# Performance work log

Measured on AMD Instinct MI355X. Metric: run time of the kernel, lower is better.

Reference implementation:

```python
import jax, jax.numpy as jnp
import numpy as np

N_GRAPHS = 64

def setup_inputs() -> dict:
    key = jax.random.key(0)
    ks = jax.random.split(key, 8)
    N, E, H = 50000, 600000, 128
    x = jax.random.normal(ks[0], (N, 2), dtype=jnp.float32)
    edge_index = jax.random.randint(ks[1], (2, E), 0, N, dtype=jnp.int64)
    batch = jnp.sort(jax.random.randint(ks[2], (N,), 0, N_GRAPHS, dtype=jnp.int64))
    s = 0.1  # keep tanh out of saturation
    return {
        'x': x,
        'edge_index': edge_index,
        'batch': batch,
        'W1': jax.random.normal(ks[3], (2, H), dtype=jnp.float32) * s,
        'b1': jnp.zeros((H,), jnp.float32),
        'W2': jax.random.normal(ks[4], (H, H), dtype=jnp.float32) * s,
        'b2': jnp.zeros((H,), jnp.float32),
        'W3': jax.random.normal(ks[5], (H, H), dtype=jnp.float32) * s,
        'b3': jnp.zeros((H,), jnp.float32),
        'Wo': jax.random.normal(ks[6], (2 * H, 41), dtype=jnp.float32) * s,
        'bo': jnp.zeros((41,), jnp.float32),
    }

def reference(x, edge_index, batch, W1, b1, W2, b2, W3, b3, Wo, bo):
    N = x.shape[0]
    src, dst = edge_index[0], edge_index[1]
    # GCN symmetric normalization with self loops: deg = in-degree + 1
    ones_e = jnp.ones(src.shape[0], dtype=x.dtype)
    deg = jax.ops.segment_sum(ones_e, dst, num_segments=N) + 1.0
    dinv = jax.lax.rsqrt(deg)                       # [N]
    edge_norm = (dinv[src] * dinv[dst])[:, None]    # [E,1]
    self_norm = (dinv * dinv)[:, None]              # [N,1]

    def gcn(h, W, b):
        h = h @ W                                   # [N,H] transform first
        agg = jax.ops.segment_sum(h[src] * edge_norm, dst, num_segments=N)
        return agg + h * self_norm + b

    h = jnp.tanh(gcn(x, W1, b1))
    h = jnp.tanh(gcn(h, W2, b2))
    h = jnp.tanh(gcn(h, W3, b3))

    # global max pool + global mean pool over graphs
    cnt = jax.ops.segment_sum(jnp.ones(N, dtype=h.dtype), batch, num_segments=N_GRAPHS)
    mx = jax.ops.segment_max(h, batch, num_segments=N_GRAPHS)
    mx = jnp.where(cnt[:, None] > 0, mx, 0.0)
    mean = jax.ops.segment_sum(h, batch, num_segments=N_GRAPHS) / jnp.maximum(cnt, 1.0)[:, None]
    pooled = jnp.concatenate([mx, mean], axis=1)    # [G, 2H]
    return jnp.tanh(pooled @ Wo + bo)               # [G, 41]
```

## Files before the change

### kernel.cpp

```cpp
#include <hip/hip_runtime.h>
#include <math.h>

#define NGRAPH 64
#define POOL_CHUNKS 32
#define SCAN_BLK 1024

typedef short short8 __attribute__((ext_vector_type(8)));
typedef float floatx4 __attribute__((ext_vector_type(4)));

__device__ inline unsigned pack_bf16x2(float a, float b) {
    unsigned ua = __float_as_uint(a);
    unsigned ub = __float_as_uint(b);
    ua = (ua + 0x7fffu + ((ua >> 16) & 1u)) >> 16;
    ub = (ub + 0x7fffu + ((ub >> 16) & 1u)) >> 16;
    return ua | (ub << 16);
}
__device__ inline unsigned short bf16_1(float a) {
    unsigned ua = __float_as_uint(a);
    return (unsigned short)((ua + 0x7fffu + ((ua >> 16) & 1u)) >> 16);
}


__global__ void count_kernel(const int* __restrict__ dst, int E, int* __restrict__ cnt) {
    int e = blockIdx.x * blockDim.x + threadIdx.x;
    if (e < E) atomicAdd(&cnt[dst[e]], 1);
}

__global__ __launch_bounds__(SCAN_BLK) void scan_phase1(const int* __restrict__ cnt,
                                                        const float* __restrict__ x,
                                                        int* __restrict__ row_ptr,
                                                        int* __restrict__ bsum,
                                                        float* __restrict__ dinv,
                                                        float2* __restrict__ y, int N) {
    __shared__ int sm[SCAN_BLK];
    int i = blockIdx.x * SCAN_BLK + threadIdx.x;
    int v = (i < N) ? cnt[i] : 0;
    if (i < N) {
        float dv = rsqrtf((float)v + 1.0f);
        dinv[i] = dv;
        float2 xv = ((const float2*)x)[i];
        y[i] = make_float2(xv.x * dv, xv.y * dv);
    }
    sm[threadIdx.x] = v;
    __syncthreads();
    for (int off = 1; off < SCAN_BLK; off <<= 1) {
        int t = (threadIdx.x >= (unsigned)off) ? sm[threadIdx.x - off] : 0;
        __syncthreads();
        sm[threadIdx.x] += t;
        __syncthreads();
    }
    if (i < N) row_ptr[i] = sm[threadIdx.x] - v;
    if (threadIdx.x == SCAN_BLK - 1) bsum[blockIdx.x] = sm[SCAN_BLK - 1];
}

__global__ __launch_bounds__(SCAN_BLK) void scan_phase2(int* __restrict__ bsum, int nb,
                                                        const int* __restrict__ batch, int N,
                                                        int* __restrict__ goff) {
    if (threadIdx.x <= NGRAPH) {
        int g = threadIdx.x;
        int lo = 0, hi = N;
        while (lo < hi) {
            int mid = (lo + hi) >> 1;
            if (batch[mid] < g) lo = mid + 1; else hi = mid;
        }
        goff[g] = lo;
    }
    __shared__ int sm[SCAN_BLK];
    int v = (threadIdx.x < (unsigned)nb) ? bsum[threadIdx.x] : 0;
    sm[threadIdx.x] = v;
    __syncthreads();
    for (int off = 1; off < SCAN_BLK; off <<= 1) {
        int t = (threadIdx.x >= (unsigned)off) ? sm[threadIdx.x - off] : 0;
        __syncthreads();
        sm[threadIdx.x] += t;
        __syncthreads();
    }
    if (threadIdx.x < (unsigned)nb) bsum[threadIdx.x] = sm[threadIdx.x] - v;
}

__global__ __launch_bounds__(SCAN_BLK) void scan_phase3(int* __restrict__ row_ptr,
                                                        const int* __restrict__ bsum,
                                                        int N, int E) {
    int i = blockIdx.x * SCAN_BLK + threadIdx.x;
    if (i < N) row_ptr[i] += bsum[blockIdx.x];
    if (i == 0) row_ptr[N] = E;
}

__global__ void fill_kernel(const int* __restrict__ src, const int* __restrict__ dst, int E,
                            const int* __restrict__ row_ptr, int* __restrict__ cnt,
                            int* __restrict__ col) {
    int e = blockIdx.x * blockDim.x + threadIdx.x;
    if (e < E) {
        int d = dst[e];
        int p = row_ptr[d] + atomicSub(&cnt[d], 1) - 1;
        col[p] = src[e];
    }
}


__global__ __launch_bounds__(256) void agg_x_kernel(const float2* __restrict__ y,
                                                    const int* __restrict__ row_ptr,
                                                    const int* __restrict__ col,
                                                    const float* __restrict__ dinv,
                                                    float2* __restrict__ z, int N) {
    int v = blockIdx.x * blockDim.x + threadIdx.x;
    if (v >= N) return;
    int s = row_ptr[v], e = row_ptr[v + 1];
    float2 a0 = y[v];
    float2 a1 = make_float2(0.f, 0.f);
    float2 a2 = make_float2(0.f, 0.f);
    float2 a3 = make_float2(0.f, 0.f);
    int j = s;
    for (; j + 4 <= e; j += 4) {
        int u0 = col[j], u1 = col[j + 1], u2 = col[j + 2], u3 = col[j + 3];
        float2 v0 = y[u0], v1 = y[u1], v2 = y[u2], v3 = y[u3];
        a0.x += v0.x; a0.y += v0.y;
        a1.x += v1.x; a1.y += v1.y;
        a2.x += v2.x; a2.y += v2.y;
        a3.x += v3.x; a3.y += v3.y;
    }
    for (; j < e; ++j) {
        float2 vv = y[col[j]];
        a0.x += vv.x; a0.y += vv.y;
    }
    float dv = dinv[v];
    z[v] = make_float2(dv * (a0.x + a1.x + a2.x + a3.x),
                       dv * (a0.y + a1.y + a2.y + a3.y));
}

__global__ __launch_bounds__(256) void transform1(const float2* __restrict__ z,
                                                  const float* __restrict__ W1,
                                                  const float* __restrict__ b1,
                                                  unsigned short* __restrict__ h, int N) {
    int tid = blockIdx.x * blockDim.x + threadIdx.x;
    int row = tid >> 5;
    if (row >= N) return;
    int q = tid & 31;
    float2 zv = z[row];
    const float4* W4 = (const float4*)W1;
    float4 w0 = W4[q];
    float4 w1 = W4[32 + q];
    float4 b = ((const float4*)b1)[q];
    float ox = tanhf(fmaf(zv.x, w0.x, fmaf(zv.y, w1.x, b.x)));
    float oy = tanhf(fmaf(zv.x, w0.y, fmaf(zv.y, w1.y, b.y)));
    float oz = tanhf(fmaf(zv.x, w0.z, fmaf(zv.y, w1.z, b.z)));
    float ow = tanhf(fmaf(zv.x, w0.w, fmaf(zv.y, w1.w, b.w)));
    uint2 pk;
    pk.x = pack_bf16x2(ox, oy);
    pk.y = pack_bf16x2(oz, ow);
    ((uint2*)h)[row * 32 + q] = pk;
}


__global__ __launch_bounds__(256) void gemm_mfma(const unsigned short* __restrict__ A,
                                                 const float* __restrict__ W,
                                                 const float* __restrict__ dinv,
                                                 unsigned short* __restrict__ t, int N) {
    __shared__ unsigned short sWt[128 * 136];
    for (int idx = threadIdx.x; idx < 16384; idx += 256) {
        int k = idx >> 7, n = idx & 127;
        sWt[n * 136 + k] = bf16_1(W[idx]);
    }
    __syncthreads();
    int w = threadIdx.x >> 6;
    int l = threadIdx.x & 63;
    int lm = l & 15;
    int k8 = (l >> 4) * 8;

    floatx4 acc[2][8];
#pragma unroll
    for (int i = 0; i < 2; ++i)
#pragma unroll
        for (int j = 0; j < 8; ++j) acc[i][j] = (floatx4){0.f, 0.f, 0.f, 0.f};

    int rowbase = blockIdx.x * 128 + w * 32;
#pragma unroll
    for (int ks = 0; ks < 4; ++ks) {
        int k0 = ks * 32 + k8;
        short8 a[2];
#pragma unroll
        for (int mt = 0; mt < 2; ++mt) {
            int r = min(rowbase + mt * 16 + lm, N - 1);
            a[mt] = *(const short8*)(A + (size_t)r * 128 + k0);
        }
#pragma unroll
        for (int nt = 0; nt < 8; ++nt) {
            short8 b = *(const short8*)(sWt + (nt * 16 + lm) * 136 + k0);
#pragma unroll
            for (int mt = 0; mt < 2; ++mt)
                acc[mt][nt] = __builtin_amdgcn_mfma_f32_16x16x32_bf16(a[mt], b, acc[mt][nt], 0, 0, 0);
        }
    }

#pragma unroll
    for (int mt = 0; mt < 2; ++mt) {
#pragma unroll
        for (int reg = 0; reg < 4; ++reg) {
            int gr = rowbase + mt * 16 + (l >> 4) * 4 + reg;
            if (gr >= N) continue;
            float dv = dinv[gr];
#pragma unroll
            for (int nt = 0; nt < 8; ++nt) {
                int c = nt * 16 + lm;
                t[(size_t)gr * 128 + c] = bf16_1(acc[mt][nt][reg] * dv);
            }
        }
    }
}


template <bool BF16OUT>
__global__ __launch_bounds__(256) void agg_kernel(const unsigned short* __restrict__ t,
                                                  const int* __restrict__ row_ptr,
                                                  const int* __restrict__ col,
                                                  const float* __restrict__ dinv,
                                                  const float* __restrict__ bias,
                                                  float* __restrict__ outF,
                                                  unsigned short* __restrict__ outB, int N) {
    int wave = threadIdx.x >> 6;
    int lane = threadIdx.x & 63;
    int half = lane >> 5;
    int q = lane & 31;
    int node = blockIdx.x * 8 + wave * 2 + half;
    if (node >= N) return;
    int s = row_ptr[node];
    int deg = row_ptr[node + 1] - s;
    const uint2* t2 = (const uint2*)t;
    float4 acc[8];
    {
        uint2 sd = t2[(size_t)node * 32 + q];
        acc[0].x = __uint_as_float(sd.x << 16);
        acc[0].y = __uint_as_float(sd.x & 0xffff0000u);
        acc[0].z = __uint_as_float(sd.y << 16);
        acc[0].w = __uint_as_float(sd.y & 0xffff0000u);
    }
#pragma unroll
    for (int i = 1; i < 8; ++i) acc[i] = make_float4(0.f, 0.f, 0.f, 0.f);
    int j = 0;
    for (; j + 8 <= deg; j += 8) {
        int u[8];
#pragma unroll
        for (int i = 0; i < 8; ++i) u[i] = col[s + j + i];
        uint2 v[8];
#pragma unroll
        for (int i = 0; i < 8; ++i) v[i] = t2[(size_t)u[i] * 32 + q];
#pragma unroll
        for (int i = 0; i < 8; ++i) {
            acc[i].x += __uint_as_float(v[i].x << 16);
            acc[i].y += __uint_as_float(v[i].x & 0xffff0000u);
            acc[i].z += __uint_as_float(v[i].y << 16);
            acc[i].w += __uint_as_float(v[i].y & 0xffff0000u);
        }
    }
    for (; j + 4 <= deg; j += 4) {
        int u[4];
#pragma unroll
        for (int i = 0; i < 4; ++i) u[i] = col[s + j + i];
        uint2 v[4];
#pragma unroll
        for (int i = 0; i < 4; ++i) v[i] = t2[(size_t)u[i] * 32 + q];
#pragma unroll
        for (int i = 0; i < 4; ++i) {
            acc[i].x += __uint_as_float(v[i].x << 16);
            acc[i].y += __uint_as_float(v[i].x & 0xffff0000u);
            acc[i].z += __uint_as_float(v[i].y << 16);
            acc[i].w += __uint_as_float(v[i].y & 0xffff0000u);
        }
    }
    for (; j < deg; ++j) {
        uint2 v = t2[(size_t)col[s + j] * 32 + q];
        acc[0].x += __uint_as_float(v.x << 16);
        acc[0].y += __uint_as_float(v.x & 0xffff0000u);
        acc[0].z += __uint_as_float(v.y << 16);
        acc[0].w += __uint_as_float(v.y & 0xffff0000u);
    }
#pragma unroll
    for (int i = 1; i < 8; ++i) {
        acc[0].x += acc[i].x; acc[0].y += acc[i].y;
        acc[0].z += acc[i].z; acc[0].w += acc[i].w;
    }
    float dv = dinv[node];
    float4 b = ((const float4*)bias)[q];
    float ox = tanhf(fmaf(dv, acc[0].x, b.x));
    float oy = tanhf(fmaf(dv, acc[0].y, b.y));
    float oz = tanhf(fmaf(dv, acc[0].z, b.z));
    float ow = tanhf(fmaf(dv, acc[0].w, b.w));
    if (BF16OUT) {
        uint2 pk;
        pk.x = pack_bf16x2(ox, oy);
        pk.y = pack_bf16x2(oz, ow);
        ((uint2*)outB)[(size_t)node * 32 + q] = pk;
    } else {
        ((float4*)outF)[(size_t)node * 32 + q] = make_float4(ox, oy, oz, ow);
    }
}


__global__ __launch_bounds__(128) void pool_partial(const float* __restrict__ h,
                                                    const int* __restrict__ goff,
                                                    float* __restrict__ part) {
    int g = blockIdx.x;
    int c = blockIdx.y;
    int j = threadIdx.x;
    int s = goff[g], e = goff[g + 1];
    int cnt = e - s;
    int per = (cnt + POOL_CHUNKS - 1) / POOL_CHUNKS;
    int ps = s + c * per;
    int pe = min(ps + per, e);
    float mx = -3.402823466e+38f, sm = 0.f;
    for (int n = ps; n < pe; ++n) {
        float v = h[(size_t)n * 128 + j];
        mx = fmaxf(mx, v);
        sm += v;
    }
    float* dst = part + ((size_t)g * POOL_CHUNKS + c) * 256;
    dst[j] = mx;
    dst[128 + j] = sm;
}

__global__ __launch_bounds__(128) void pool_final(const float* __restrict__ part,
                                                  const int* __restrict__ goff,
                                                  const float* __restrict__ Wo,
                                                  const float* __restrict__ bo,
                                                  float* __restrict__ out) {
    __shared__ float p[256];
    int g = blockIdx.x;
    int j = threadIdx.x;
    float mx = -3.402823466e+38f, sm = 0.f;
    const float* base = part + (size_t)g * POOL_CHUNKS * 256;
#pragma unroll 4
    for (int c = 0; c < POOL_CHUNKS; ++c) {
        mx = fmaxf(mx, base[c * 256 + j]);
        sm += base[c * 256 + 128 + j];
    }
    int cnt = goff[g + 1] - goff[g];
    p[j] = (cnt > 0) ? mx : 0.f;
    p[128 + j] = sm / fmaxf((float)cnt, 1.f);
    __syncthreads();
    if (j < 41) {
        float acc = bo[j];
        for (int k = 0; k < 256; ++k) acc = fmaf(p[k], Wo[k * 41 + j], acc);
        out[g * 41 + j] = tanhf(acc);
    }
}


extern "C" void kernel_launch(void* const* d_in, const int* in_sizes, int n_in,
                              void* d_out, int out_size, void* d_ws, size_t ws_size,
                              hipStream_t stream) {
    const float* x   = (const float*)d_in[0];
    const int*   ei  = (const int*)d_in[1];
    const int* batch = (const int*)d_in[2];
    const float* W1  = (const float*)d_in[3];
    const float* b1  = (const float*)d_in[4];
    const float* W2  = (const float*)d_in[5];
    const float* b2  = (const float*)d_in[6];
    const float* W3  = (const float*)d_in[7];
    const float* b3  = (const float*)d_in[8];
    const float* Wo  = (const float*)d_in[9];
    const float* bo  = (const float*)d_in[10];
    float* outp = (float*)d_out;

    int N = in_sizes[2];
    int E = in_sizes[1] / 2;
    const int* src = ei;
    const int* dst = ei + E;

    char* p = (char*)d_ws;
    auto alloc = [&](size_t bytes) -> char* {
        char* q = p;
        p += (bytes + 255) & ~(size_t)255;
        return q;
    };
    unsigned short* t  = (unsigned short*)alloc((size_t)N * 128 * 2);
    unsigned short* hb = (unsigned short*)alloc((size_t)N * 128 * 2);
    float* h3     = (float*)alloc((size_t)N * 128 * 4);
    float* dinv   = (float*)alloc((size_t)N * 4);
    int*   cnt    = (int*)alloc((size_t)N * 4);
    int*   rowp   = (int*)alloc((size_t)(N + 1) * 4);
    int*   col    = (int*)alloc((size_t)E * 4);
    int*   goff   = (int*)alloc(65 * 4);
    float* part   = (float*)alloc((size_t)NGRAPH * POOL_CHUNKS * 256 * 4);
    float2* y     = (float2*)alloc((size_t)N * 8);
    float2* z     = (float2*)alloc((size_t)N * 8);
    int nscan = (N + SCAN_BLK - 1) / SCAN_BLK;
    int*   bsum   = (int*)alloc((size_t)nscan * 4);

    hipMemsetAsync(cnt, 0, (size_t)N * 4, stream);

    count_kernel<<<(E + 255) / 256, 256, 0, stream>>>(dst, E, cnt);
    scan_phase1<<<nscan, SCAN_BLK, 0, stream>>>(cnt, x, rowp, bsum, dinv, y, N);
    scan_phase2<<<1, SCAN_BLK, 0, stream>>>(bsum, nscan, batch, N, goff);
    scan_phase3<<<nscan, SCAN_BLK, 0, stream>>>(rowp, bsum, N, E);
    fill_kernel<<<(E + 255) / 256, 256, 0, stream>>>(src, dst, E, rowp, cnt, col);

    agg_x_kernel<<<(N + 255) / 256, 256, 0, stream>>>(y, rowp, col, dinv, z, N);
    transform1<<<((size_t)N * 32 + 255) / 256, 256, 0, stream>>>(z, W1, b1, hb, N);
    gemm_mfma<<<(N + 127) / 128, 256, 0, stream>>>(hb, W2, dinv, t, N);
    agg_kernel<true><<<(N + 7) / 8, 256, 0, stream>>>(t, rowp, col, dinv, b2, nullptr, hb, N);
    gemm_mfma<<<(N + 127) / 128, 256, 0, stream>>>(hb, W3, dinv, t, N);
    agg_kernel<false><<<(N + 7) / 8, 256, 0, stream>>>(t, rowp, col, dinv, b3, h3, nullptr, N);

    dim3 pgrid(NGRAPH, POOL_CHUNKS);
    pool_partial<<<pgrid, 128, 0, stream>>>(h3, goff, part);
    pool_final<<<NGRAPH, 128, 0, stream>>>(part, goff, Wo, bo, outp);
}
```

Before: 277.7 us.

## Prepack bf16 transposed weights once and widen aggregation gathers to 16B

A new packWt kernel converts W2 and W3 to bf16 and transposes them once per call. Each gemm_mfma block then copies the packed weights into shared memory with 16-byte loads, instead of every block converting and transposing the full fp32 matrix element by element. The aggregation kernel now uses 16 lanes per node with uint4 (8 bf16) gathers and 4 accumulators instead of 32 lanes with uint2 gathers and 8 accumulators. This halves lanes per row, so a wave covers more nodes and issues fewer, wider memory transactions. The cost is one extra launch and more registers per lane.

After: 273.0 us. Within noise of the previous version (-1.7%).

```diff
diff --git a/kernel.cpp b/kernel.cpp
--- a/kernel.cpp
+++ b/kernel.cpp
@@ -94,6 +94,31 @@
         int d = dst[e];
         int p = row_ptr[d] + atomicSub(&cnt[d], 1) - 1;
         col[p] = src[e];
+    }
+}
+
+
+__global__ __launch_bounds__(256) void packWt(const float* __restrict__ W2,
+                                              const float* __restrict__ W3,
+                                              unsigned* __restrict__ Wt2,
+                                              unsigned* __restrict__ Wt3) {
+    int b = blockIdx.x;
+    const float* W = (b < 16) ? W2 : W3;
+    unsigned* Wt = (b < 16) ? Wt2 : Wt3;
+    b &= 15;
+    int bk = b & 3, bn = b >> 2;
+    __shared__ float s[32][33];
+    int tx = threadIdx.x & 31, ty = threadIdx.x >> 5;
+#pragma unroll
+    for (int r = 0; r < 4; ++r)
+        s[r * 8 + ty][tx] = W[(bk * 32 + r * 8 + ty) * 128 + bn * 32 + tx];
+    __syncthreads();
+    int t16 = threadIdx.x & 15, tn = threadIdx.x >> 4;
+#pragma unroll
+    for (int pass = 0; pass < 2; ++pass) {
+        int nl = pass * 16 + tn;
+        unsigned pk = pack_bf16x2(s[2 * t16][nl], s[2 * t16 + 1][nl]);
+        Wt[(bn * 32 + nl) * 64 + bk * 16 + t16] = pk;
     }
 }
 
@@ -153,19 +178,21 @@
 
 
 __global__ __launch_bounds__(256) void gemm_mfma(const unsigned short* __restrict__ A,
-                                                 const float* __restrict__ W,
+                                                 const unsigned* __restrict__ Wt,
                                                  const float* __restrict__ dinv,
                                                  unsigned short* __restrict__ t, int N) {
-    __shared__ unsigned short sWt[128 * 136];
-    for (int idx = threadIdx.x; idx < 16384; idx += 256) {
-        int k = idx >> 7, n = idx & 127;
-        sWt[n * 136 + k] = bf16_1(W[idx]);
+    __shared__ unsigned sW[128 * 68];
+    const uint4* Wt4 = (const uint4*)Wt;
+    for (int i = threadIdx.x; i < 2048; i += 256) {
+        int n = i >> 4, c = i & 15;
+        *(uint4*)&sW[n * 68 + c * 4] = Wt4[i];
     }
     __syncthreads();
     int w = threadIdx.x >> 6;
     int l = threadIdx.x & 63;
     int lm = l & 15;
-    int k8 = (l >> 4) * 8;
+    int q4 = l >> 4;
+    int k8 = q4 * 8;
 
     floatx4 acc[2][8];
 #pragma unroll
@@ -185,7 +212,7 @@
         }
 #pragma unroll
         for (int nt = 0; nt < 8; ++nt) {
-            short8 b = *(const short8*)(sWt + (nt * 16 + lm) * 136 + k0);
+            short8 b = *(const short8*)&sW[(nt * 16 + lm) * 68 + ks * 16 + q4 * 4];
 #pragma unroll
             for (int mt = 0; mt < 2; ++mt)
                 acc[mt][nt] = __builtin_amdgcn_mfma_f32_16x16x32_bf16(a[mt], b, acc[mt][nt], 0, 0, 0);
@@ -196,7 +223,7 @@
     for (int mt = 0; mt < 2; ++mt) {
 #pragma unroll
         for (int reg = 0; reg < 4; ++reg) {
-            int gr = rowbase + mt * 16 + (l >> 4) * 4 + reg;
+            int gr = rowbase + mt * 16 + q4 * 4 + reg;
             if (gr >= N) continue;
             float dv = dinv[gr];
 #pragma unroll
@@ -219,79 +246,86 @@
                                                   unsigned short* __restrict__ outB, int N) {
     int wave = threadIdx.x >> 6;
     int lane = threadIdx.x & 63;
-    int half = lane >> 5;
-    int q = lane & 31;
-    int node = blockIdx.x * 8 + wave * 2 + half;
+    int sub  = lane >> 4;
+    int q    = lane & 15;
+    int node = blockIdx.x * 16 + wave * 4 + sub;
     if (node >= N) return;
     int s = row_ptr[node];
     int deg = row_ptr[node + 1] - s;
-    const uint2* t2 = (const uint2*)t;
-    float4 acc[8];
+    const uint4* t4 = (const uint4*)t;
+    float acc[4][8];
     {
-        uint2 sd = t2[(size_t)node * 32 + q];
-        acc[0].x = __uint_as_float(sd.x << 16);
-        acc[0].y = __uint_as_float(sd.x & 0xffff0000u);
-        acc[0].z = __uint_as_float(sd.y << 16);
-        acc[0].w = __uint_as_float(sd.y & 0xffff0000u);
-    }
-#pragma unroll
-    for (int i = 1; i < 8; ++i) acc[i] = make_float4(0.f, 0.f, 0.f, 0.f);
+        uint4 sd = t4[(size_t)node * 16 + q];
+        acc[0][0] = __uint_as_float(sd.x << 16);
+        acc[0][1] = __uint_as_float(sd.x & 0xffff0000u);
+        acc[0][2] = __uint_as_float(sd.y << 16);
+        acc[0][3] = __uint_as_float(sd.y & 0xffff0000u);
+        acc[0][4] = __uint_as_float(sd.z << 16);
+        acc[0][5] = __uint_as_float(sd.z & 0xffff0000u);
+        acc[0][6] = __uint_as_float(sd.w << 16);
+        acc[0][7] = __uint_as_float(sd.w & 0xffff0000u);
+    }
+#pragma unroll
+    for (int i = 1; i < 4; ++i)
+#pragma unroll
+        for (int k = 0; k < 8; ++k) acc[i][k] = 0.f;
     int j = 0;
-    for (; j + 8 <= deg; j += 8) {
-        int u[8];
-#pragma unroll
-        for (int i = 0; i < 8; ++i) u[i] = col[s + j + i];
-        uint2 v[8];
-#pragma unroll
-        for (int i = 0; i < 8; ++i) v[i] = t2[(size_t)u[i] * 32 + q];
-#pragma unroll
-        for (int i = 0; i < 8; ++i) {
-            acc[i].x += __uint_as_float(v[i].x << 16);
-            acc[i].y += __uint_as_float(v[i].x & 0xffff0000u);
-            acc[i].z += __uint_as_float(v[i].y << 16);
-            acc[i].w += __uint_as_float(v[i].y & 0xffff0000u);
-        }
-    }
     for (; j + 4 <= deg; j += 4) {
         int u[4];
 #pragma unroll
         for (int i = 0; i < 4; ++i) u[i] = col[s + j + i];
-        uint2 v[4];
-#pragma unroll
-        for (int i = 0; i < 4; ++i) v[i] = t2[(size_t)u[i] * 32 + q];
+        uint4 v[4];
+#pragma unroll
+        for (int i = 0; i < 4; ++i) v[i] = t4[(size_t)u[i] * 16 + q];
 #pragma unroll
         for (int i = 0; i < 4; ++i) {
-            acc[i].x += __uint_as_float(v[i].x << 16);
-            acc[i].y += __uint_as_float(v[i].x & 0xffff0000u);
-            acc[i].z += __uint_as_float(v[i].y << 16);
-            acc[i].w += __uint_as_float(v[i].y & 0xffff0000u);
+            acc[i][0] += __uint_as_float(v[i].x << 16);
+            acc[i][1] += __uint_as_float(v[i].x & 0xffff0000u);
+            acc[i][2] += __uint_as_float(v[i].y << 16);
+            acc[i][3] += __uint_as_float(v[i].y & 0xffff0000u);
+            acc[i][4] += __uint_as_float(v[i].z << 16);
+            acc[i][5] += __uint_as_float(v[i].z & 0xffff0000u);
+            acc[i][6] += __uint_as_float(v[i].w << 16);
+            acc[i][7] += __uint_as_float(v[i].w & 0xffff0000u);
         }
     }
     for (; j < deg; ++j) {
-        uint2 v = t2[(size_t)col[s + j] * 32 + q];
-        acc[0].x += __uint_as_float(v.x << 16);
-        acc[0].y += __uint_as_float(v.x & 0xffff0000u);
-        acc[0].z += __uint_as_float(v.y << 16);
-        acc[0].w += __uint_as_float(v.y & 0xffff0000u);
-    }
-#pragma unroll
-    for (int i = 1; i < 8; ++i) {
-        acc[0].x += acc[i].x; acc[0].y += acc[i].y;
-        acc[0].z += acc[i].z; acc[0].w += acc[i].w;
-    }
+        uint4 v = t4[(size_t)col[s + j] * 16 + q];
+        acc[0][0] += __uint_as_float(v.x << 16);
+        acc[0][1] += __uint_as_float(v.x & 0xffff0000u);
+        acc[0][2] += __uint_as_float(v.y << 16);
+        acc[0][3] += __uint_as_float(v.y & 0xffff0000u);
+        acc[0][4] += __uint_as_float(v.z << 16);
+        acc[0][5] += __uint_as_float(v.z & 0xffff0000u);
+        acc[0][6] += __uint_as_float(v.w << 16);
+        acc[0][7] += __uint_as_float(v.w & 0xffff0000u);
+    }
+#pragma unroll
+    for (int i = 1; i < 4; ++i)
+#pragma unroll
+        for (int k = 0; k < 8; ++k) acc[0][k] += acc[i][k];
     float dv = dinv[node];
-    float4 b = ((const float4*)bias)[q];
-    float ox = tanhf(fmaf(dv, acc[0].x, b.x));
-    float oy = tanhf(fmaf(dv, acc[0].y, b.y));
-    float oz = tanhf(fmaf(dv, acc[0].z, b.z));
-    float ow = tanhf(fmaf(dv, acc[0].w, b.w));
+    float4 b0 = ((const float4*)bias)[2 * q];
+    float4 b1 = ((const float4*)bias)[2 * q + 1];
+    float o[8];
+    o[0] = tanhf(fmaf(dv, acc[0][0], b0.x));
+    o[1] = tanhf(fmaf(dv, acc[0][1], b0.y));
+    o[2] = tanhf(fmaf(dv, acc[0][2], b0.z));
+    o[3] = tanhf(fmaf(dv, acc[0][3], b0.w));
+    o[4] = tanhf(fmaf(dv, acc[0][4], b1.x));
+    o[5] = tanhf(fmaf(dv, acc[0][5], b1.y));
+    o[6] = tanhf(fmaf(dv, acc[0][6], b1.z));
+    o[7] = tanhf(fmaf(dv, acc[0][7], b1.w));
     if (BF16OUT) {
-        uint2 pk;
-        pk.x = pack_bf16x2(ox, oy);
-        pk.y = pack_bf16x2(oz, ow);
-        ((uint2*)outB)[(size_t)node * 32 + q] = pk;
+        uint4 pk;
+        pk.x = pack_bf16x2(o[0], o[1]);
+        pk.y = pack_bf16x2(o[2], o[3]);
+        pk.z = pack_bf16x2(o[4], o[5]);
+        pk.w = pack_bf16x2(o[6], o[7]);
+        ((uint4*)outB)[(size_t)node * 16 + q] = pk;
     } else {
-        ((float4*)outF)[(size_t)node * 32 + q] = make_float4(ox, oy, oz, ow);
+        ((float4*)outF)[(size_t)node * 32 + 2 * q]     = make_float4(o[0], o[1], o[2], o[3]);
+        ((float4*)outF)[(size_t)node * 32 + 2 * q + 1] = make_float4(o[4], o[5], o[6], o[7]);
     }
 }
 
@@ -383,11 +417,14 @@
     float* part   = (float*)alloc((size_t)NGRAPH * POOL_CHUNKS * 256 * 4);
     float2* y     = (float2*)alloc((size_t)N * 8);
     float2* z     = (float2*)alloc((size_t)N * 8);
+    unsigned* Wt2 = (unsigned*)alloc(128 * 64 * 4);
+    unsigned* Wt3 = (unsigned*)alloc(128 * 64 * 4);
     int nscan = (N + SCAN_BLK - 1) / SCAN_BLK;
     int*   bsum   = (int*)alloc((size_t)nscan * 4);
 
     hipMemsetAsync(cnt, 0, (size_t)N * 4, stream);
 
+    packWt<<<32, 256, 0, stream>>>(W2, W3, Wt2, Wt3);
     count_kernel<<<(E + 255) / 256, 256, 0, stream>>>(dst, E, cnt);
     scan_phase1<<<nscan, SCAN_BLK, 0, stream>>>(cnt, x, rowp, bsum, dinv, y, N);
     scan_phase2<<<1, SCAN_BLK, 0, stream>>>(bsum, nscan, batch, N, goff);
@@ -396,10 +433,10 @@
 
     agg_x_kernel<<<(N + 255) / 256, 256, 0, stream>>>(y, rowp, col, dinv, z, N);
     transform1<<<((size_t)N * 32 + 255) / 256, 256, 0, stream>>>(z, W1, b1, hb, N);
-    gemm_mfma<<<(N + 127) / 128, 256, 0, stream>>>(hb, W2, dinv, t, N);
-    agg_kernel<true><<<(N + 7) / 8, 256, 0, stream>>>(t, rowp, col, dinv, b2, nullptr, hb, N);
-    gemm_mfma<<<(N + 127) / 128, 256, 0, stream>>>(hb, W3, dinv, t, N);
-    agg_kernel<false><<<(N + 7) / 8, 256, 0, stream>>>(t, rowp, col, dinv, b3, h3, nullptr, N);
+    gemm_mfma<<<(N + 127) / 128, 256, 0, stream>>>(hb, Wt2, dinv, t, N);
+    agg_kernel<true><<<(N + 15) / 16, 256, 0, stream>>>(t, rowp, col, dinv, b2, nullptr, hb, N);
+    gemm_mfma<<<(N + 127) / 128, 256, 0, stream>>>(hb, Wt3, dinv, t, N);
+    agg_kernel<false><<<(N + 15) / 16, 256, 0, stream>>>(t, rowp, col, dinv, b3, h3, nullptr, N);
 
     dim3 pgrid(NGRAPH, POOL_CHUNKS);
     pool_partial<<<pgrid, 128, 0, stream>>>(h3, goff, part);
```
